# Kernel optimization log

Measured on AMD Instinct MI355X. Metric: run time of the kernel, lower is better.

The kernel has to match this reference:

```python
import jax, jax.numpy as jnp
import numpy as np

B, L, G, K, D = 8, 4096, 64, 16, 64
N = G * K  # 1024 slots
EPS = 1e-5


def setup_inputs() -> dict:
    key = jax.random.key(0)
    ks = jax.random.split(key, 12)
    def w(k, shape):
        fan_in = shape[-1]
        return jax.random.normal(k, shape, jnp.float32) / np.sqrt(fan_in)
    return {
        "X": jax.random.normal(ks[0], (B, L, D), jnp.float32),
        "S": jax.random.normal(ks[1], (B, N, D), jnp.float32),
        "Wg": w(ks[2], (G, 2 * D)),
        "Ws": w(ks[3], (K, 2 * D)),
        "mw0": w(ks[4], (2 * D, 2 * D)), "mb0": jnp.zeros((2 * D,), jnp.float32),
        "mw1": w(ks[5], (D, 2 * D)),     "mb1": jnp.zeros((D,), jnp.float32),
        "gw0": w(ks[6], (D, 2 * D)),     "gb0": jnp.zeros((D,), jnp.float32),
        "gw1": w(ks[7], (1, D)),         "gb1": jnp.zeros((1,), jnp.float32),
        "uw0": w(ks[8], (2 * D, 2 * D)), "ub0": jnp.zeros((2 * D,), jnp.float32),
        "uw1": w(ks[9], (D, 2 * D)),     "ub1": jnp.zeros((D,), jnp.float32),
        "ln_w": jnp.ones((D,), jnp.float32),
        "ln_b": jnp.zeros((D,), jnp.float32),
    }


def _gelu(x):
    return jax.nn.gelu(x, approximate=False)  # torch nn.GELU default = exact erf


def reference(X, S, Wg, Ws, mw0, mb0, mw1, mb1, gw0, gb0, gw1, gb1,
              uw0, ub0, uw1, ub1, ln_w, ln_b):
    # state summary (detached in torch)
    S_sum = jnp.mean(jax.lax.stop_gradient(S), axis=1, keepdims=True)  # [B,1,D]
    XS = jnp.concatenate([X, jnp.broadcast_to(S_sum, X.shape)], axis=-1)  # [B,L,2D]

    msg = _gelu(XS @ mw0.T + mb0) @ mw1.T + mb1                    # [B,L,D]
    gate = jax.nn.sigmoid(_gelu(XS @ gw0.T + gb0) @ gw1.T + gb1)   # [B,L,1]
    gated_msg = msg * gate

    # eval-mode hard WTA routing: argmax one-hot == scatter index
    g_idx = jnp.argmax(XS @ Wg.T, axis=-1)  # [B,L]
    s_idx = jnp.argmax(XS @ Ws.T, axis=-1)  # [B,L]
    slot = g_idx * K + s_idx                # flat slot index in [0,N)

    # scatter-add gated messages into slot buckets (== bmm with one-hot)
    flat_idx = (jnp.arange(B, dtype=slot.dtype)[:, None] * N + slot).reshape(-1)
    incoming = jax.ops.segment_sum(gated_msg.reshape(B * L, D), flat_idx,
                                   num_segments=B * N).reshape(B, N, D)

    upd_in = jnp.concatenate([S, incoming], axis=-1)               # [B,N,2D]
    S_new = S + (_gelu(upd_in @ uw0.T + ub0) @ uw1.T + ub1)

    mu = jnp.mean(S_new, axis=-1, keepdims=True)
    var = jnp.mean((S_new - mu) ** 2, axis=-1, keepdims=True)
    return (S_new - mu) * jax.lax.rsqrt(var + EPS) * ln_w + ln_b
```

## Files before the change

### kernel.cpp

```cpp
#include <hip/hip_runtime.h>
#include <math.h>

#define B 8
#define L 4096
#define D 64
#define TD 128
#define G 64
#define KS 16
#define NSLOT 1024
#define EPS 1e-5f
#define TB 8

#define OFF_SSUM 0
#define OFF_WGT  512
#define OFF_WST  8704
#define OFF_UW0T 10752
#define OFF_UW1T 27136
#define OFF_MW0B 35328
#define OFF_MW1B 43520
#define OFF_GW0B 47616
#define OFF_SLOT 51712
#define OFF_INC  84480

typedef __attribute__((ext_vector_type(8))) short short8;
typedef __attribute__((ext_vector_type(4))) float f32x4;

__device__ __forceinline__ float gelu_exact(float x) {
    return 0.5f * x * (1.0f + erff(x * 0.70710678118654752f));
}

__device__ __forceinline__ unsigned short f2bf(float f) {
    unsigned u = __float_as_uint(f);
    u += 0x7FFFu + ((u >> 16) & 1u);
    return (unsigned short)(u >> 16);
}

__global__ __launch_bounds__(256) void prep_kernel(
    const float* __restrict__ S, const float* __restrict__ Wg,
    const float* __restrict__ Ws, const float* __restrict__ mw0,
    const float* __restrict__ mw1, const float* __restrict__ gw0,
    const float* __restrict__ uw0, const float* __restrict__ uw1,
    float* __restrict__ ws)
{
    int blk = blockIdx.x;
    if (blk < 264) {
        int idx = blk * 256 + threadIdx.x;
        unsigned short* wsu = (unsigned short*)ws;
        if (idx < 8192) {
            int k = idx >> 6, g = idx & 63;
            ws[OFF_WGT + idx] = Wg[g * TD + k];
        } else if (idx < 10240) {
            int r = idx - 8192; int k = r >> 4, s = r & 15;
            ws[OFF_WST + r] = Ws[s * TD + k];
        } else if (idx < 26624) {
            int r = idx - 10240; int k = r >> 7, j = r & 127;
            ws[OFF_UW0T + r] = uw0[j * TD + k];
        } else if (idx < 34816) {
            int r = idx - 26624; int k = r >> 6, j = r & 63;
            ws[OFF_UW1T + r] = uw1[j * TD + k];
        } else if (idx < 51200) {
            int r = idx - 34816;
            int e = r & 7, l = (r >> 3) & 63, ks = (r >> 9) & 3, jt = r >> 11;
            int j = jt * 16 + (l & 15); int k = ks * 32 + (l >> 4) * 8 + e;
            wsu[OFF_MW0B * 2 + r] = f2bf(mw0[j * TD + k]);
        } else if (idx < 59392) {
            int r = idx - 51200;
            int e = r & 7, l = (r >> 3) & 63, ks = (r >> 9) & 3, jt = r >> 11;
            int j = jt * 16 + (l & 15); int k = ks * 32 + (l >> 4) * 8 + e;
            wsu[OFF_MW1B * 2 + r] = f2bf(mw1[j * TD + k]);
        } else if (idx < 67584) {
            int r = idx - 59392;
            int e = r & 7, l = (r >> 3) & 63, ks = (r >> 9) & 3, jt = r >> 11;
            int j = jt * 16 + (l & 15); int k = ks * 32 + (l >> 4) * 8 + e;
            wsu[OFF_GW0B * 2 + r] = f2bf(gw0[j * TD + k]);
        }
    } else {
        int b = blk - 264;
        int d = threadIdx.x;
        if (d < D) {
            const float* Sp = S + (size_t)b * NSLOT * D + d;
            float acc = 0.f;
            for (int n0 = 0; n0 < NSLOT; n0 += 16) {
                float v[16];
                #pragma unroll
                for (int u = 0; u < 16; ++u) v[u] = Sp[(size_t)(n0 + u) * D];
                #pragma unroll
                for (int u = 0; u < 16; ++u) acc += v[u];
            }
            ws[OFF_SSUM + b * D + d] = acc * (1.0f / NSLOT);
        }
    }
}

__global__ __launch_bounds__(256) void routing_kernel(
    const float* __restrict__ X, float* __restrict__ ws)
{
    __shared__ float xs[2][TD][TB];
    __shared__ float lg[2][G][TB];
    __shared__ float ls[2][KS][TB];

    const int half = threadIdx.x >> 7;
    const int tid  = threadIdx.x & 127;
    const int t0 = blockIdx.x * 16 + half * TB;
    const int b  = t0 / L;
    const int l0 = t0 % L;

    for (int idx = tid; idx < TB * D; idx += 128) {
        int t = idx >> 6, d = idx & 63;
        xs[half][d][t]     = X[((size_t)(b * L + l0 + t)) * D + d];
        xs[half][d + D][t] = ws[OFF_SSUM + b * D + d];
    }
    __syncthreads();

    {
        if (tid < G) {
            int g = tid;
            float acc[TB];
            #pragma unroll
            for (int t = 0; t < TB; ++t) acc[t] = 0.f;
            const float* wp = ws + OFF_WGT + g;
            #pragma unroll 4
            for (int k = 0; k < TD; ++k) {
                float w = wp[k * G];
                float4 a = *(const float4*)&xs[half][k][0];
                float4 c = *(const float4*)&xs[half][k][4];
                acc[0] += w * a.x; acc[1] += w * a.y; acc[2] += w * a.z; acc[3] += w * a.w;
                acc[4] += w * c.x; acc[5] += w * c.y; acc[6] += w * c.z; acc[7] += w * c.w;
            }
            #pragma unroll
            for (int t = 0; t < TB; ++t) lg[half][g][t] = acc[t];
        } else if (tid < G + KS) {
            int s = tid - G;
            float acc[TB];
            #pragma unroll
            for (int t = 0; t < TB; ++t) acc[t] = 0.f;
            const float* wp = ws + OFF_WST + s;
            #pragma unroll 4
            for (int k = 0; k < TD; ++k) {
                float w = wp[k * KS];
                float4 a = *(const float4*)&xs[half][k][0];
                float4 c = *(const float4*)&xs[half][k][4];
                acc[0] += w * a.x; acc[1] += w * a.y; acc[2] += w * a.z; acc[3] += w * a.w;
                acc[4] += w * c.x; acc[5] += w * c.y; acc[6] += w * c.z; acc[7] += w * c.w;
            }
            #pragma unroll
            for (int t = 0; t < TB; ++t) ls[half][s][t] = acc[t];
        }
    }
    __syncthreads();

    if (tid < TB) {
        int t = tid;
        int bg = 0; float bv = lg[half][0][t];
        for (int g = 1; g < G; ++g) { float v = lg[half][g][t]; if (v > bv) { bv = v; bg = g; } }
        int bs = 0; float sv = ls[half][0][t];
        for (int s = 1; s < KS; ++s) { float v = ls[half][s][t]; if (v > sv) { sv = v; bs = s; } }
        ((int*)(ws + OFF_SLOT))[t0 + t] = bg * KS + bs;
    }
}

__global__ __launch_bounds__(256) void msg_kernel(
    const float* __restrict__ X,
    const float* __restrict__ mb0, const float* __restrict__ mb1,
    const float* __restrict__ gb0, const float* __restrict__ gw1,
    const float* __restrict__ gb1, float* __restrict__ ws)
{
    __shared__ __align__(16) unsigned short xsl[64 * 136];
    __shared__ __align__(16) unsigned short hhl[64 * 136];
    __shared__ float msgl[64 * 68];
    __shared__ float ghl[64 * 68];
    __shared__ float gatel[64];
    __shared__ int   slotl[64];

    const int tid  = threadIdx.x;
    const int tok0 = blockIdx.x * 64;
    const int b    = tok0 >> 12;

    if (tid < 64) slotl[tid] = ((const int*)(ws + OFF_SLOT))[tok0 + tid];

    {
        int t = tid >> 2, q = tid & 3;
        unsigned short tmp[32];
        if (q < 2) {
            const float* Xp = X + (size_t)(tok0 + t) * D + q * 32;
            #pragma unroll
            for (int u = 0; u < 8; ++u) {
                float4 v = *(const float4*)(Xp + u * 4);
                tmp[u*4+0] = f2bf(v.x); tmp[u*4+1] = f2bf(v.y);
                tmp[u*4+2] = f2bf(v.z); tmp[u*4+3] = f2bf(v.w);
            }
        } else {
            const float* Sp = ws + OFF_SSUM + b * D + (q - 2) * 32;
            #pragma unroll
            for (int u = 0; u < 32; ++u) tmp[u] = f2bf(Sp[u]);
        }
        #pragma unroll
        for (int s = 0; s < 4; ++s)
            *(short8*)&xsl[t * 136 + (q * 4 + s) * 8] = *(const short8*)&tmp[s * 8];
    }
    __syncthreads();

    const int w  = tid >> 6;
    const int l  = tid & 63;
    const int lr = l & 15;
    const int lk = l >> 4;
    const unsigned short* wsu = (const unsigned short*)ws;

    {
        f32x4 acc[2][4];
        #pragma unroll
        for (int a_ = 0; a_ < 2; ++a_)
            #pragma unroll
            for (int b_ = 0; b_ < 4; ++b_) acc[a_][b_] = (f32x4){0.f, 0.f, 0.f, 0.f};

        for (int ks = 0; ks < 4; ++ks) {
            short8 a[4];
            #pragma unroll
            for (int tt = 0; tt < 4; ++tt)
                a[tt] = *(const short8*)&xsl[(tt * 16 + lr) * 136 + (ks * 4 + lk) * 8];
            #pragma unroll
            for (int jt2 = 0; jt2 < 2; ++jt2) {
                int jt = w * 2 + jt2;
                short8 bb = *(const short8*)&wsu[OFF_MW0B * 2 + ((jt * 4 + ks) * 64 + l) * 8];
                #pragma unroll
                for (int tt = 0; tt < 4; ++tt)
                    acc[jt2][tt] = __builtin_amdgcn_mfma_f32_16x16x32_bf16(a[tt], bb, acc[jt2][tt], 0, 0, 0);
            }
        }
        #pragma unroll
        for (int jt2 = 0; jt2 < 2; ++jt2) {
            int j = w * 32 + jt2 * 16 + lr;
            float bias = mb0[j];
            #pragma unroll
            for (int tt = 0; tt < 4; ++tt) {
                #pragma unroll
                for (int r = 0; r < 4; ++r) {
                    int t = tt * 16 + lk * 4 + r;
                    hhl[t * 136 + j] = f2bf(gelu_exact(acc[jt2][tt][r] + bias));
                }
            }
        }
    }
    __syncthreads();

    {
        f32x4 acc[2][4];
        #pragma unroll
        for (int a_ = 0; a_ < 2; ++a_)
            #pragma unroll
            for (int b_ = 0; b_ < 4; ++b_) acc[a_][b_] = (f32x4){0.f, 0.f, 0.f, 0.f};

        const unsigned short* srcA = (w < 2) ? hhl : xsl;
        const int wb   = (w < 2) ? w : (w - 2);
        const int boff = (w < 2) ? OFF_MW1B * 2 : OFF_GW0B * 2;

        for (int ks = 0; ks < 4; ++ks) {
            short8 a[4];
            #pragma unroll
            for (int tt = 0; tt < 4; ++tt)
                a[tt] = *(const short8*)&srcA[(tt * 16 + lr) * 136 + (ks * 4 + lk) * 8];
            #pragma unroll
            for (int jt2 = 0; jt2 < 2; ++jt2) {
                int jt = wb * 2 + jt2;
                short8 bb = *(const short8*)&wsu[boff + ((jt * 4 + ks) * 64 + l) * 8];
                #pragma unroll
                for (int tt = 0; tt < 4; ++tt)
                    acc[jt2][tt] = __builtin_amdgcn_mfma_f32_16x16x32_bf16(a[tt], bb, acc[jt2][tt], 0, 0, 0);
            }
        }
        if (w < 2) {
            #pragma unroll
            for (int jt2 = 0; jt2 < 2; ++jt2) {
                int j = w * 32 + jt2 * 16 + lr;
                float bias = mb1[j];
                #pragma unroll
                for (int tt = 0; tt < 4; ++tt)
                    #pragma unroll
                    for (int r = 0; r < 4; ++r) {
                        int t = tt * 16 + lk * 4 + r;
                        msgl[t * 68 + j] = acc[jt2][tt][r] + bias;
                    }
            }
        } else {
            #pragma unroll
            for (int jt2 = 0; jt2 < 2; ++jt2) {
                int j = wb * 32 + jt2 * 16 + lr;
                float bias = gb0[j];
                #pragma unroll
                for (int tt = 0; tt < 4; ++tt)
                    #pragma unroll
                    for (int r = 0; r < 4; ++r) {
                        int t = tt * 16 + lk * 4 + r;
                        ghl[t * 68 + j] = gelu_exact(acc[jt2][tt][r] + bias);
                    }
            }
        }
    }
    __syncthreads();

    if (tid < 64) {
        float acc = gb1[0];
        for (int jj = 0; jj < D; ++jj) acc += ghl[tid * 68 + jj] * gw1[jj];
        gatel[tid] = 1.0f / (1.0f + expf(-acc));
    }
    __syncthreads();

    float* inc = ws + OFF_INC;
    #pragma unroll
    for (int i = tid; i < 64 * D; i += 256) {
        int t = i >> 6, d = i & 63;
        atomicAdd(&inc[((size_t)(b * NSLOT + slotl[t])) * D + d], msgl[t * 68 + d] * gatel[t]);
    }
}

__global__ __launch_bounds__(256) void update_kernel(
    const float* __restrict__ S,
    const float* __restrict__ ub0, const float* __restrict__ ub1,
    const float* __restrict__ ln_w, const float* __restrict__ ln_b,
    const float* __restrict__ ws, float* __restrict__ out)
{
    __shared__ float row[TD][TB];
    __shared__ float pb[2][TD][TB];
    __shared__ float uu[TD][TB];
    __shared__ float pc[4][D][TB];
    __shared__ float sn[D][TB];
    __shared__ float mu_s[TB], rs_s[TB];

    const int r0 = blockIdx.x * TB;
    const int tid = threadIdx.x;

    for (int idx = tid; idx < TB * D; idx += 256) {
        int t = idx >> 6, d = idx & 63;
        size_t g = (size_t)(r0 + t) * D + d;
        row[d][t]     = S[g];
        row[d + D][t] = ws[OFF_INC + g];
    }
    __syncthreads();

    {
        int j = tid & 127, kh = tid >> 7;
        float acc[TB];
        #pragma unroll
        for (int t = 0; t < TB; ++t) acc[t] = 0.f;
        const float* wp = ws + OFF_UW0T + (size_t)kh * 64 * TD + j;
        #pragma unroll 4
        for (int k = 0; k < 64; ++k) {
            float w = wp[k * TD];
            float4 a = *(const float4*)&row[kh * 64 + k][0];
            float4 c = *(const float4*)&row[kh * 64 + k][4];
            acc[0] += w * a.x; acc[1] += w * a.y; acc[2] += w * a.z; acc[3] += w * a.w;
            acc[4] += w * c.x; acc[5] += w * c.y; acc[6] += w * c.z; acc[7] += w * c.w;
        }
        #pragma unroll
        for (int t = 0; t < TB; ++t) pb[kh][j][t] = acc[t];
    }
    __syncthreads();
    for (int idx = tid; idx < TD * TB; idx += 256) {
        int j = idx >> 3, t = idx & 7;
        uu[j][t] = gelu_exact(pb[0][j][t] + pb[1][j][t] + ub0[j]);
    }
    __syncthreads();

    {
        int d = tid & 63, kq = tid >> 6;
        float acc[TB];
        #pragma unroll
        for (int t = 0; t < TB; ++t) acc[t] = 0.f;
        const float* wp = ws + OFF_UW1T + (size_t)kq * 32 * D + d;
        #pragma unroll 4
        for (int k = 0; k < 32; ++k) {
            float w = wp[k * D];
            float4 a = *(const float4*)&uu[kq * 32 + k][0];
            float4 c = *(const float4*)&uu[kq * 32 + k][4];
            acc[0] += w * a.x; acc[1] += w * a.y; acc[2] += w * a.z; acc[3] += w * a.w;
            acc[4] += w * c.x; acc[5] += w * c.y; acc[6] += w * c.z; acc[7] += w * c.w;
        }
        #pragma unroll
        for (int t = 0; t < TB; ++t) pc[kq][d][t] = acc[t];
    }
    __syncthreads();
    for (int idx = tid; idx < D * TB; idx += 256) {
        int d = idx >> 3, t = idx & 7;
        sn[d][t] = S[(size_t)(r0 + t) * D + d] + ub1[d]
                 + pc[0][d][t] + pc[1][d][t] + pc[2][d][t] + pc[3][d][t];
    }
    __syncthreads();

    if (tid < TB) {
        int t = tid;
        float m = 0.f;
        for (int d = 0; d < D; ++d) m += sn[d][t];
        m *= (1.0f / D);
        float v = 0.f;
        for (int d = 0; d < D; ++d) { float dd = sn[d][t] - m; v += dd * dd; }
        v *= (1.0f / D);
        mu_s[t] = m;
        rs_s[t] = rsqrtf(v + EPS);
    }
    __syncthreads();

    for (int idx = tid; idx < TB * D; idx += 256) {
        int t = idx >> 6, d = idx & 63;
        out[(size_t)(r0 + t) * D + d] = (sn[d][t] - mu_s[t]) * rs_s[t] * ln_w[d] + ln_b[d];
    }
}

extern "C" void kernel_launch(void* const* d_in, const int* in_sizes, int n_in,
                              void* d_out, int out_size, void* d_ws, size_t ws_size,
                              hipStream_t stream)
{
    const float* X    = (const float*)d_in[0];
    const float* S    = (const float*)d_in[1];
    const float* Wg   = (const float*)d_in[2];
    const float* Ws   = (const float*)d_in[3];
    const float* mw0  = (const float*)d_in[4];
    const float* mb0  = (const float*)d_in[5];
    const float* mw1  = (const float*)d_in[6];
    const float* mb1  = (const float*)d_in[7];
    const float* gw0  = (const float*)d_in[8];
    const float* gb0  = (const float*)d_in[9];
    const float* gw1  = (const float*)d_in[10];
    const float* gb1  = (const float*)d_in[11];
    const float* uw0  = (const float*)d_in[12];
    const float* ub0  = (const float*)d_in[13];
    const float* uw1  = (const float*)d_in[14];
    const float* ub1  = (const float*)d_in[15];
    const float* ln_w = (const float*)d_in[16];
    const float* ln_b = (const float*)d_in[17];

    float* ws  = (float*)d_ws;
    float* out = (float*)d_out;

    hipMemsetAsync(ws + OFF_INC, 0, (size_t)B * NSLOT * D * sizeof(float), stream);

    prep_kernel<<<272, 256, 0, stream>>>(S, Wg, Ws, mw0, mw1, gw0, uw0, uw1, ws);
    routing_kernel<<<(B * L) / 16, 256, 0, stream>>>(X, ws);
    msg_kernel<<<(B * L) / 64, 256, 0, stream>>>(X, mb0, mb1, gb0, gw1, gb1, ws);
    update_kernel<<<(B * NSLOT) / TB, 256, 0, stream>>>(S, ub0, ub1, ln_w, ln_b, ws, out);
}
```

Baseline: 182.4 us.

## Move routing and update GEMMs to bf16 MFMA with fp32 recheck for near-ties

Routing logits are now computed with bf16 MFMA on 64-token tiles, and the top-two gap is tracked for each argmax. Tokens whose margin falls below a threshold are recomputed exactly in fp32 so the slot choice stays correct. The slot update MLP also moves from scalar fp32 FMAs to bf16 MFMA over 32-row tiles, with the weights pre-packed into fragment layout in the prep kernel. This trades fp32 precision in the update path for matrix-core throughput and fewer blocks. Routing correctness depends on the margin heuristic catching every near-tie.

```diff
diff --git a/kernel.cpp b/kernel.cpp
--- a/kernel.cpp
+++ b/kernel.cpp
@@ -9,18 +9,20 @@
 #define KS 16
 #define NSLOT 1024
 #define EPS 1e-5f
-#define TB 8
+#define MARGIN 0.04f
 
 #define OFF_SSUM 0
 #define OFF_WGT  512
 #define OFF_WST  8704
-#define OFF_UW0T 10752
-#define OFF_UW1T 27136
-#define OFF_MW0B 35328
-#define OFF_MW1B 43520
-#define OFF_GW0B 47616
-#define OFF_SLOT 51712
-#define OFF_INC  84480
+#define OFF_MW0B 10752
+#define OFF_MW1B 18944
+#define OFF_GW0B 23040
+#define OFF_WGB  27136
+#define OFF_WSB  31232
+#define OFF_UW0B 32256
+#define OFF_UW1B 40448
+#define OFF_SLOT 44544
+#define OFF_INC  77312
 
 typedef __attribute__((ext_vector_type(8))) short short8;
 typedef __attribute__((ext_vector_type(4))) float f32x4;
@@ -33,6 +35,12 @@
     unsigned u = __float_as_uint(f);
     u += 0x7FFFu + ((u >> 16) & 1u);
     return (unsigned short)(u >> 16);
+}
+
+__device__ __forceinline__ void fragmap(int r, int& j, int& k) {
+    int e = r & 7, l = (r >> 3) & 63, ks = (r >> 9) & 3, jt = r >> 11;
+    j = jt * 16 + (l & 15);
+    k = ks * 32 + (l >> 4) * 8 + e;
 }
 
 __global__ __launch_bounds__(256) void prep_kernel(
@@ -43,39 +51,40 @@
     float* __restrict__ ws)
 {
     int blk = blockIdx.x;
-    if (blk < 264) {
+    if (blk < 304) {
         int idx = blk * 256 + threadIdx.x;
         unsigned short* wsu = (unsigned short*)ws;
+        int j, k;
         if (idx < 8192) {
-            int k = idx >> 6, g = idx & 63;
-            ws[OFF_WGT + idx] = Wg[g * TD + k];
+            int kk = idx >> 6, g = idx & 63;
+            ws[OFF_WGT + idx] = Wg[g * TD + kk];
         } else if (idx < 10240) {
-            int r = idx - 8192; int k = r >> 4, s = r & 15;
-            ws[OFF_WST + r] = Ws[s * TD + k];
+            int r = idx - 8192; int kk = r >> 4, s = r & 15;
+            ws[OFF_WST + r] = Ws[s * TD + kk];
         } else if (idx < 26624) {
-            int r = idx - 10240; int k = r >> 7, j = r & 127;
-            ws[OFF_UW0T + r] = uw0[j * TD + k];
+            int r = idx - 10240; fragmap(r, j, k);
+            wsu[OFF_MW0B * 2 + r] = f2bf(mw0[j * TD + k]);
         } else if (idx < 34816) {
-            int r = idx - 26624; int k = r >> 6, j = r & 63;
-            ws[OFF_UW1T + r] = uw1[j * TD + k];
+            int r = idx - 26624; fragmap(r, j, k);
+            wsu[OFF_MW1B * 2 + r] = f2bf(mw1[j * TD + k]);
+        } else if (idx < 43008) {
+            int r = idx - 34816; fragmap(r, j, k);
+            wsu[OFF_GW0B * 2 + r] = f2bf(gw0[j * TD + k]);
         } else if (idx < 51200) {
-            int r = idx - 34816;
-            int e = r & 7, l = (r >> 3) & 63, ks = (r >> 9) & 3, jt = r >> 11;
-            int j = jt * 16 + (l & 15); int k = ks * 32 + (l >> 4) * 8 + e;
-            wsu[OFF_MW0B * 2 + r] = f2bf(mw0[j * TD + k]);
-        } else if (idx < 59392) {
-            int r = idx - 51200;
-            int e = r & 7, l = (r >> 3) & 63, ks = (r >> 9) & 3, jt = r >> 11;
-            int j = jt * 16 + (l & 15); int k = ks * 32 + (l >> 4) * 8 + e;
-            wsu[OFF_MW1B * 2 + r] = f2bf(mw1[j * TD + k]);
-        } else if (idx < 67584) {
-            int r = idx - 59392;
-            int e = r & 7, l = (r >> 3) & 63, ks = (r >> 9) & 3, jt = r >> 11;
-            int j = jt * 16 + (l & 15); int k = ks * 32 + (l >> 4) * 8 + e;
-            wsu[OFF_GW0B * 2 + r] = f2bf(gw0[j * TD + k]);
+            int r = idx - 43008; fragmap(r, j, k);
+            wsu[OFF_WGB * 2 + r] = f2bf(Wg[j * TD + k]);
+        } else if (idx < 53248) {
+            int r = idx - 51200; fragmap(r, j, k);
+            wsu[OFF_WSB * 2 + r] = f2bf(Ws[j * TD + k]);
+        } else if (idx < 69632) {
+            int r = idx - 53248; fragmap(r, j, k);
+            wsu[OFF_UW0B * 2 + r] = f2bf(uw0[j * TD + k]);
+        } else if (idx < 77824) {
+            int r = idx - 69632; fragmap(r, j, k);
+            wsu[OFF_UW1B * 2 + r] = f2bf(uw1[j * TD + k]);
         }
     } else {
-        int b = blk - 264;
+        int b = blk - 304;
         int d = threadIdx.x;
         if (d < D) {
             const float* Sp = S + (size_t)b * NSLOT * D + d;
@@ -95,68 +104,142 @@
 __global__ __launch_bounds__(256) void routing_kernel(
     const float* __restrict__ X, float* __restrict__ ws)
 {
-    __shared__ float xs[2][TD][TB];
-    __shared__ float lg[2][G][TB];
-    __shared__ float ls[2][KS][TB];
-
-    const int half = threadIdx.x >> 7;
-    const int tid  = threadIdx.x & 127;
-    const int t0 = blockIdx.x * 16 + half * TB;
-    const int b  = t0 / L;
-    const int l0 = t0 % L;
-
-    for (int idx = tid; idx < TB * D; idx += 128) {
-        int t = idx >> 6, d = idx & 63;
-        xs[half][d][t]     = X[((size_t)(b * L + l0 + t)) * D + d];
-        xs[half][d + D][t] = ws[OFF_SSUM + b * D + d];
-    }
-    __syncthreads();
+    __shared__ __align__(16) unsigned short xsl[64 * 136];
+    __shared__ float lgl[64][85];
+    __shared__ int   slotl[64];
+    __shared__ unsigned char flags[64];
+    __shared__ int   flist[64];
+    __shared__ int   flagcnt;
+
+    const int tid  = threadIdx.x;
+    const int tok0 = blockIdx.x * 64;
+    const int b    = tok0 >> 12;
+
+    if (tid == 0) flagcnt = 0;
 
     {
-        if (tid < G) {
-            int g = tid;
-            float acc[TB];
-            #pragma unroll
-            for (int t = 0; t < TB; ++t) acc[t] = 0.f;
-            const float* wp = ws + OFF_WGT + g;
-            #pragma unroll 4
-            for (int k = 0; k < TD; ++k) {
-                float w = wp[k * G];
-                float4 a = *(const float4*)&xs[half][k][0];
-                float4 c = *(const float4*)&xs[half][k][4];
-                acc[0] += w * a.x; acc[1] += w * a.y; acc[2] += w * a.z; acc[3] += w * a.w;
-                acc[4] += w * c.x; acc[5] += w * c.y; acc[6] += w * c.z; acc[7] += w * c.w;
-            }
-            #pragma unroll
-            for (int t = 0; t < TB; ++t) lg[half][g][t] = acc[t];
-        } else if (tid < G + KS) {
-            int s = tid - G;
-            float acc[TB];
-            #pragma unroll
-            for (int t = 0; t < TB; ++t) acc[t] = 0.f;
-            const float* wp = ws + OFF_WST + s;
-            #pragma unroll 4
-            for (int k = 0; k < TD; ++k) {
-                float w = wp[k * KS];
-                float4 a = *(const float4*)&xs[half][k][0];
-                float4 c = *(const float4*)&xs[half][k][4];
-                acc[0] += w * a.x; acc[1] += w * a.y; acc[2] += w * a.z; acc[3] += w * a.w;
-                acc[4] += w * c.x; acc[5] += w * c.y; acc[6] += w * c.z; acc[7] += w * c.w;
-            }
-            #pragma unroll
-            for (int t = 0; t < TB; ++t) ls[half][s][t] = acc[t];
-        }
-    }
-    __syncthreads();
-
-    if (tid < TB) {
+        int t = tid >> 2, q = tid & 3;
+        unsigned short tmp[32];
+        if (q < 2) {
+            const float* Xp = X + (size_t)(tok0 + t) * D + q * 32;
+            #pragma unroll
+            for (int u = 0; u < 8; ++u) {
+                float4 v = *(const float4*)(Xp + u * 4);
+                tmp[u*4+0] = f2bf(v.x); tmp[u*4+1] = f2bf(v.y);
+                tmp[u*4+2] = f2bf(v.z); tmp[u*4+3] = f2bf(v.w);
+            }
+        } else {
+            const float* Sp = ws + OFF_SSUM + b * D + (q - 2) * 32;
+            #pragma unroll
+            for (int u = 0; u < 32; ++u) tmp[u] = f2bf(Sp[u]);
+        }
+        #pragma unroll
+        for (int s = 0; s < 4; ++s)
+            *(short8*)&xsl[t * 136 + (q * 4 + s) * 8] = *(const short8*)&tmp[s * 8];
+    }
+    __syncthreads();
+
+    const int w  = tid >> 6;
+    const int l  = tid & 63;
+    const int lr = l & 15;
+    const int lk = l >> 4;
+    const unsigned short* wsu = (const unsigned short*)ws;
+
+    if (w < 2) {
+        f32x4 acc[2][4];
+        #pragma unroll
+        for (int c2 = 0; c2 < 2; ++c2)
+            #pragma unroll
+            for (int tt = 0; tt < 4; ++tt) acc[c2][tt] = (f32x4){0.f,0.f,0.f,0.f};
+        for (int ks = 0; ks < 4; ++ks) {
+            short8 a[4];
+            #pragma unroll
+            for (int tt = 0; tt < 4; ++tt)
+                a[tt] = *(const short8*)&xsl[(tt * 16 + lr) * 136 + (ks * 4 + lk) * 8];
+            #pragma unroll
+            for (int c2 = 0; c2 < 2; ++c2) {
+                int jt = w * 2 + c2;
+                short8 bb = *(const short8*)&wsu[OFF_WGB * 2 + ((jt * 4 + ks) * 64 + l) * 8];
+                #pragma unroll
+                for (int tt = 0; tt < 4; ++tt)
+                    acc[c2][tt] = __builtin_amdgcn_mfma_f32_16x16x32_bf16(a[tt], bb, acc[c2][tt], 0, 0, 0);
+            }
+        }
+        #pragma unroll
+        for (int c2 = 0; c2 < 2; ++c2) {
+            int j = (w * 2 + c2) * 16 + lr;
+            #pragma unroll
+            for (int tt = 0; tt < 4; ++tt)
+                #pragma unroll
+                for (int r = 0; r < 4; ++r)
+                    lgl[tt * 16 + lk * 4 + r][j] = acc[c2][tt][r];
+        }
+    } else {
+        f32x4 acc[2];
+        acc[0] = (f32x4){0.f,0.f,0.f,0.f}; acc[1] = (f32x4){0.f,0.f,0.f,0.f};
+        int ttb = (w - 2) * 2;
+        for (int ks = 0; ks < 4; ++ks) {
+            short8 a0 = *(const short8*)&xsl[((ttb    ) * 16 + lr) * 136 + (ks * 4 + lk) * 8];
+            short8 a1 = *(const short8*)&xsl[((ttb + 1) * 16 + lr) * 136 + (ks * 4 + lk) * 8];
+            short8 bb = *(const short8*)&wsu[OFF_WSB * 2 + (ks * 64 + l) * 8];
+            acc[0] = __builtin_amdgcn_mfma_f32_16x16x32_bf16(a0, bb, acc[0], 0, 0, 0);
+            acc[1] = __builtin_amdgcn_mfma_f32_16x16x32_bf16(a1, bb, acc[1], 0, 0, 0);
+        }
+        #pragma unroll
+        for (int tt2 = 0; tt2 < 2; ++tt2)
+            #pragma unroll
+            for (int r = 0; r < 4; ++r)
+                lgl[(ttb + tt2) * 16 + lk * 4 + r][64 + lr] = acc[tt2][r];
+    }
+    __syncthreads();
+
+    if (tid < 64) {
         int t = tid;
-        int bg = 0; float bv = lg[half][0][t];
-        for (int g = 1; g < G; ++g) { float v = lg[half][g][t]; if (v > bv) { bv = v; bg = g; } }
-        int bs = 0; float sv = ls[half][0][t];
-        for (int s = 1; s < KS; ++s) { float v = ls[half][s][t]; if (v > sv) { sv = v; bs = s; } }
-        ((int*)(ws + OFF_SLOT))[t0 + t] = bg * KS + bs;
-    }
+        float bv = lgl[t][0], g2 = -1e30f; int bg = 0;
+        for (int g = 1; g < G; ++g) {
+            float v = lgl[t][g];
+            if (v > bv) { g2 = bv; bv = v; bg = g; } else if (v > g2) g2 = v;
+        }
+        float sv = lgl[t][64], s2 = -1e30f; int bs = 0;
+        for (int s = 1; s < KS; ++s) {
+            float v = lgl[t][64 + s];
+            if (v > sv) { s2 = sv; sv = v; bs = s; } else if (v > s2) s2 = v;
+        }
+        bool fl = (bv - g2 < MARGIN) || (sv - s2 < MARGIN);
+        flags[t] = fl;
+        slotl[t] = bg * KS + bs;
+        if (fl) { int i = atomicAdd(&flagcnt, 1); flist[i] = t; }
+    }
+    __syncthreads();
+
+    int nf = flagcnt;
+    for (int fi = 0; fi < nf; ++fi) {
+        int t = flist[fi];
+        if (tid < 80) {
+            bool isg = tid < 64;
+            const float* wp = isg ? (ws + OFF_WGT + tid) : (ws + OFF_WST + (tid - 64));
+            int stride = isg ? G : KS;
+            const float* xp = X + (size_t)(tok0 + t) * D;
+            const float* sp = ws + OFF_SSUM + b * D;
+            float acc = 0.f;
+            #pragma unroll 8
+            for (int k = 0; k < 64; ++k) acc += wp[k * stride] * xp[k];
+            #pragma unroll 8
+            for (int k = 0; k < 64; ++k) acc += wp[(64 + k) * stride] * sp[k];
+            lgl[t][tid] = acc;
+        }
+        __syncthreads();
+    }
+    if (tid < 64 && flags[tid]) {
+        int t = tid;
+        float bv = lgl[t][0]; int bg = 0;
+        for (int g = 1; g < G; ++g) { float v = lgl[t][g]; if (v > bv) { bv = v; bg = g; } }
+        float sv = lgl[t][64]; int bs = 0;
+        for (int s = 1; s < KS; ++s) { float v = lgl[t][64 + s]; if (v > sv) { sv = v; bs = s; } }
+        slotl[t] = bg * KS + bs;
+    }
+    __syncthreads();
+    if (tid < 64) ((int*)(ws + OFF_SLOT))[tok0 + tid] = slotl[tid];
 }
 
 __global__ __launch_bounds__(256) void msg_kernel(
@@ -319,89 +402,106 @@
     const float* __restrict__ ln_w, const float* __restrict__ ln_b,
     const float* __restrict__ ws, float* __restrict__ out)
 {
-    __shared__ float row[TD][TB];
-    __shared__ float pb[2][TD][TB];
-    __shared__ float uu[TD][TB];
-    __shared__ float pc[4][D][TB];
-    __shared__ float sn[D][TB];
-    __shared__ float mu_s[TB], rs_s[TB];
-
-    const int r0 = blockIdx.x * TB;
+    __shared__ __align__(16) unsigned short rowl[32 * 136];
+    __shared__ __align__(16) unsigned short uul[32 * 136];
+    __shared__ float s32[32][69];
+    __shared__ float dl[32][69];
+    __shared__ float mu_s[32], rs_s[32];
+
+    const int r0  = blockIdx.x * 32;
     const int tid = threadIdx.x;
 
-    for (int idx = tid; idx < TB * D; idx += 256) {
+    for (int idx = tid; idx < 32 * D; idx += 256) {
         int t = idx >> 6, d = idx & 63;
         size_t g = (size_t)(r0 + t) * D + d;
-        row[d][t]     = S[g];
-        row[d + D][t] = ws[OFF_INC + g];
-    }
-    __syncthreads();
+        float sv = S[g], iv = ws[OFF_INC + g];
+        s32[t][d] = sv;
+        rowl[t * 136 + d]     = f2bf(sv);
+        rowl[t * 136 + D + d] = f2bf(iv);
+    }
+    __syncthreads();
+
+    const int w  = tid >> 6;
+    const int l  = tid & 63;
+    const int lr = l & 15;
+    const int lk = l >> 4;
+    const unsigned short* wsu = (const unsigned short*)ws;
 
     {
-        int j = tid & 127, kh = tid >> 7;
-        float acc[TB];
-        #pragma unroll
-        for (int t = 0; t < TB; ++t) acc[t] = 0.f;
-        const float* wp = ws + OFF_UW0T + (size_t)kh * 64 * TD + j;
-        #pragma unroll 4
-        for (int k = 0; k < 64; ++k) {
-            float w = wp[k * TD];
-            float4 a = *(const float4*)&row[kh * 64 + k][0];
-            float4 c = *(const float4*)&row[kh * 64 + k][4];
-            acc[0] += w * a.x; acc[1] += w * a.y; acc[2] += w * a.z; acc[3] += w * a.w;
-            acc[4] += w * c.x; acc[5] += w * c.y; acc[6] += w * c.z; acc[7] += w * c.w;
-        }
-        #pragma unroll
-        for (int t = 0; t < TB; ++t) pb[kh][j][t] = acc[t];
-    }
-    __syncthreads();
-    for (int idx = tid; idx < TD * TB; idx += 256) {
-        int j = idx >> 3, t = idx & 7;
-        uu[j][t] = gelu_exact(pb[0][j][t] + pb[1][j][t] + ub0[j]);
+        f32x4 acc[2][2];
+        #pragma unroll
+        for (int c2 = 0; c2 < 2; ++c2) { acc[c2][0] = (f32x4){0.f,0.f,0.f,0.f}; acc[c2][1] = (f32x4){0.f,0.f,0.f,0.f}; }
+        for (int ks = 0; ks < 4; ++ks) {
+            short8 a[2];
+            #pragma unroll
+            for (int tt = 0; tt < 2; ++tt)
+                a[tt] = *(const short8*)&rowl[(tt * 16 + lr) * 136 + (ks * 4 + lk) * 8];
+            #pragma unroll
+            for (int c2 = 0; c2 < 2; ++c2) {
+                int jt = w * 2 + c2;
+                short8 bb = *(const short8*)&wsu[OFF_UW0B * 2 + ((jt * 4 + ks) * 64 + l) * 8];
+                #pragma unroll
+                for (int tt = 0; tt < 2; ++tt)
+                    acc[c2][tt] = __builtin_amdgcn_mfma_f32_16x16x32_bf16(a[tt], bb, acc[c2][tt], 0, 0, 0);
+            }
+        }
+        #pragma unroll
+        for (int c2 = 0; c2 < 2; ++c2) {
+            int j = (w * 2 + c2) * 16 + lr;
+            float bias = ub0[j];
+            #pragma unroll
+            for (int tt = 0; tt < 2; ++tt)
+                #pragma unroll
+                for (int r = 0; r < 4; ++r) {
+                    int t = tt * 16 + lk * 4 + r;
+                    uul[t * 136 + j] = f2bf(gelu_exact(acc[c2][tt][r] + bias));
+                }
+        }
     }
     __syncthreads();
 
     {
-        int d = tid & 63, kq = tid >> 6;
-        float acc[TB];
-        #pragma unroll
-        for (int t = 0; t < TB; ++t) acc[t] = 0.f;
-        const float* wp = ws + OFF_UW1T + (size_t)kq * 32 * D + d;
-        #pragma unroll 4
-        for (int k = 0; k < 32; ++k) {
-            float w = wp[k * D];
-            float4 a = *(const float4*)&uu[kq * 32 + k][0];
-            float4 c = *(const float4*)&uu[kq * 32 + k][4];
-            acc[0] += w * a.x; acc[1] += w * a.y; acc[2] += w * a.z; acc[3] += w * a.w;
-            acc[4] += w * c.x; acc[5] += w * c.y; acc[6] += w * c.z; acc[7] += w * c.w;
-        }
-        #pragma unroll
-        for (int t = 0; t < TB; ++t) pc[kq][d][t] = acc[t];
-    }
-    __syncthreads();
-    for (int idx = tid; idx < D * TB; idx += 256) {
-        int d = idx >> 3, t = idx & 7;
-        sn[d][t] = S[(size_t)(r0 + t) * D + d] + ub1[d]
-                 + pc[0][d][t] + pc[1][d][t] + pc[2][d][t] + pc[3][d][t];
-    }
-    __syncthreads();
-
-    if (tid < TB) {
+        f32x4 acc[2];
+        acc[0] = (f32x4){0.f,0.f,0.f,0.f}; acc[1] = (f32x4){0.f,0.f,0.f,0.f};
+        for (int ks = 0; ks < 4; ++ks) {
+            short8 a[2];
+            #pragma unroll
+            for (int tt = 0; tt < 2; ++tt)
+                a[tt] = *(const short8*)&uul[(tt * 16 + lr) * 136 + (ks * 4 + lk) * 8];
+            short8 bb = *(const short8*)&wsu[OFF_UW1B * 2 + ((w * 4 + ks) * 64 + l) * 8];
+            #pragma unroll
+            for (int tt = 0; tt < 2; ++tt)
+                acc[tt] = __builtin_amdgcn_mfma_f32_16x16x32_bf16(a[tt], bb, acc[tt], 0, 0, 0);
+        }
+        int j = w * 16 + lr;
+        float bias = ub1[j];
+        #pragma unroll
+        for (int tt = 0; tt < 2; ++tt)
+            #pragma unroll
+            for (int r = 0; r < 4; ++r) {
+                int t = tt * 16 + lk * 4 + r;
+                dl[t][j] = acc[tt][r] + bias;
+            }
+    }
+    __syncthreads();
+
+    if (tid < 32) {
         int t = tid;
         float m = 0.f;
-        for (int d = 0; d < D; ++d) m += sn[d][t];
+        for (int d = 0; d < D; ++d) m += s32[t][d] + dl[t][d];
         m *= (1.0f / D);
         float v = 0.f;
-        for (int d = 0; d < D; ++d) { float dd = sn[d][t] - m; v += dd * dd; }
+        for (int d = 0; d < D; ++d) { float dd = s32[t][d] + dl[t][d] - m; v += dd * dd; }
         v *= (1.0f / D);
         mu_s[t] = m;
         rs_s[t] = rsqrtf(v + EPS);
     }
     __syncthreads();
 
-    for (int idx = tid; idx < TB * D; idx += 256) {
+    for (int idx = tid; idx < 32 * D; idx += 256) {
         int t = idx >> 6, d = idx & 63;
-        out[(size_t)(r0 + t) * D + d] = (sn[d][t] - mu_s[t]) * rs_s[t] * ln_w[d] + ln_b[d];
+        out[(size_t)(r0 + t) * D + d] =
+            (s32[t][d] + dl[t][d] - mu_s[t]) * rs_s[t] * ln_w[d] + ln_b[d];
     }
 }
 
@@ -433,8 +533,8 @@
 
     hipMemsetAsync(ws + OFF_INC, 0, (size_t)B * NSLOT * D * sizeof(float), stream);
 
-    prep_kernel<<<272, 256, 0, stream>>>(S, Wg, Ws, mw0, mw1, gw0, uw0, uw1, ws);
-    routing_kernel<<<(B * L) / 16, 256, 0, stream>>>(X, ws);
+    prep_kernel<<<312, 256, 0, stream>>>(S, Wg, Ws, mw0, mw1, gw0, uw0, uw1, ws);
+    routing_kernel<<<(B * L) / 64, 256, 0, stream>>>(X, ws);
     msg_kernel<<<(B * L) / 64, 256, 0, stream>>>(X, mb0, mb1, gb0, gw1, gb1, ws);
-    update_kernel<<<(B * NSLOT) / TB, 256, 0, stream>>>(S, ub0, ub1, ln_w, ln_b, ws, out);
-}
+    update_kernel<<<(B * NSLOT) / 32, 256, 0, stream>>>(S, ub0, ub1, ln_w, ln_b, ws, out);
+}
```

Result: slower. 209.2 us (+14.7%).
